# Optimization experiments

Measured on AMD Instinct MI355X. Metric: run time of the kernel, lower is better.

Reference implementation:

```python
import jax, jax.numpy as jnp
import numpy as np
from jax.scipy.special import logsumexp

EPS = 1e-12  # torch F.normalize eps
SINKHORN_ITERS = 3


def _l2norm(a, axis):
    n = jnp.sqrt(jnp.sum(a * a, axis=axis, keepdims=True))
    return a / jnp.maximum(n, EPS)


def _log_optimal_transport(scores, alpha, iters):
    # scores: [B, m, n]; alpha: scalar dust-bin param
    b, m, n = scores.shape
    bins = jnp.broadcast_to(alpha, (b, 1, n)).astype(scores.dtype)
    Z = jnp.concatenate([scores, bins], axis=1)  # [B, m+1, n]
    norm = -np.log(float(m + n))
    log_mu = jnp.asarray(
        np.concatenate([np.full(m, norm), [np.log(float(n - m)) + norm]]),
        scores.dtype,
    )  # [m+1]
    log_nu = jnp.full((n,), norm, scores.dtype)
    u = jnp.zeros((b, m + 1), scores.dtype)
    v = jnp.zeros((b, n), scores.dtype)
    for _ in range(iters):
        u = log_mu[None, :] - logsumexp(Z + v[:, None, :], axis=2)
        v = log_nu[None, :] - logsumexp(Z + u[:, :, None], axis=1)
    return Z + u[:, :, None] + v[:, None, :] - norm


def _forward(x, t, tw1, tb1, tw2, tb2, cw1, cb1, cw2, cb2, sw1, sb1, sw2, sb2, dust_bin):
    B, C = x.shape[0], x.shape[1]
    xf = x.reshape(B, C, -1)  # [B, C, N], 1x1 convs act per-location
    # cluster features f: [B, l, N]
    h = jax.nn.relu(jnp.einsum('oc,bcn->bon', cw1, xf) + cb1[None, :, None])
    f = jnp.einsum('oc,bcn->bon', cw2, h) + cb2[None, :, None]
    # global token: [B, g]
    tok = jax.nn.relu(t @ tw1.T + tb1) @ tw2.T + tb2
    # assignment scores p: [B, m, N]
    hs = jax.nn.relu(jnp.einsum('oc,bcn->bon', sw1, xf) + sb1[None, :, None])
    p = jnp.einsum('oc,bcn->bon', sw2, hs) + sb2[None, :, None]
    Z = _log_optimal_transport(p, dust_bin, SINKHORN_ITERS)
    P = jnp.exp(Z)[:, :-1, :]  # drop dust bin row -> [B, m, N]
    # VLAD-style aggregation: the repeat/multiply/sum is just a batched matmul
    agg = jnp.einsum('bln,bmn->blm', f, P)  # [B, l, m]
    agg = _l2norm(agg, axis=1).reshape(B, -1)  # intra-normalize over l, flatten l-major
    out = jnp.concatenate([_l2norm(tok, axis=-1), agg], axis=-1)
    return _l2norm(out, axis=-1)


def setup_inputs() -> dict:
    key = jax.random.key(0)
    ks = jax.random.split(key, 14)
    B, C, H, W = 64, 768, 32, 32
    L, M, G, HID = 128, 64, 256, 512

    def p(k, shape):
        return jax.random.normal(k, shape, jnp.float32) * 0.02

    return {
        'x': jax.random.normal(ks[0], (B, C, H, W), jnp.float32),
        't': jax.random.normal(ks[1], (B, C), jnp.float32),
        'tw1': p(ks[2], (HID, C)), 'tb1': jnp.zeros((HID,), jnp.float32),
        'tw2': p(ks[3], (G, HID)), 'tb2': jnp.zeros((G,), jnp.float32),
        'cw1': p(ks[4], (HID, C)), 'cb1': jnp.zeros((HID,), jnp.float32),
        'cw2': p(ks[5], (L, HID)), 'cb2': jnp.zeros((L,), jnp.float32),
        'sw1': p(ks[6], (HID, C)), 'sb1': jnp.zeros((HID,), jnp.float32),
        'sw2': p(ks[7], (M, HID)), 'sb2': jnp.zeros((M,), jnp.float32),
        'dust_bin': jnp.asarray(1.0, jnp.float32),
    }


def reference(x, t, tw1, tb1, tw2, tb2, cw1, cb1, cw2, cb2, sw1, sb1, sw2, sb2, dust_bin):
    return _forward(x, t, tw1, tb1, tw2, tb2, cw1, cb1, cw2, cb2, sw1, sb1, sw2, sb2, dust_bin)
```

## Files before the change

### kernel.cpp

```cpp
#include <hip/hip_runtime.h>
#include <math.h>


#define B_SZ   64
#define C_IN   768
#define N_LOC  1024
#define HID    512
#define L_DIM  128
#define M_DIM  64
#define G_DIM  256

typedef unsigned short u16;
typedef __bf16 bf16x8 __attribute__((ext_vector_type(8)));
typedef float f32x4 __attribute__((ext_vector_type(4)));

typedef const __attribute__((address_space(1))) void* gptr_t;
typedef __attribute__((address_space(3))) void* sptr_t;

__device__ __forceinline__ void load_lds16(const void* g, void* l) {
    __builtin_amdgcn_global_load_lds((gptr_t)g, (sptr_t)l, 16, 0, 0);
}

__device__ __forceinline__ u16 f2bf(float f) {
    unsigned u = __float_as_uint(f);
    u += 0x7fffu + ((u >> 16) & 1u);
    return (u16)(u >> 16);
}
__device__ __forceinline__ float bf2f(u16 h) {
    return __uint_as_float(((unsigned)h) << 16);
}

__device__ __forceinline__ float waveReduceSum(float v) {
#pragma unroll
    for (int off = 32; off > 0; off >>= 1) v += __shfl_xor(v, off, 64);
    return v;
}

__global__ __launch_bounds__(256) void prep_weights(
        const float* __restrict__ cw1, const float* __restrict__ sw1,
        const float* __restrict__ cw2, const float* __restrict__ sw2,
        u16* __restrict__ cw1p, u16* __restrict__ sw1p,
        u16* __restrict__ cw2p, u16* __restrict__ sw2p) {
    const int q = blockIdx.x * 256 + threadIdx.x;
    const float* src;
    u16* dst;
    if (q < 98304) {
        int path = q / 49152, r = q % 49152;
        int kt = r / 2048, kc = (r / 512) & 3, c = r & 511;
        src = (path ? sw1 : cw1) + (size_t)c * C_IN + kt * 32 + kc * 8;
        dst = (path ? sw1p : cw1p) + (size_t)r * 8;
    } else {
        int q2 = q - 98304;
        int path = (q2 >= 8192) ? 1 : 0;
        int r = q2 - (path ? 8192 : 0);
        int S2 = path ? M_DIM : L_DIM;
        int k2 = r / (4 * S2), kc = (r / S2) & 3, c = r % S2;
        src = (path ? sw2 : cw2) + (size_t)c * HID + k2 * 32 + kc * 8;
        dst = (path ? sw2p : cw2p) + (size_t)r * 8;
    }
    float4 v0 = *(const float4*)(src);
    float4 v1 = *(const float4*)(src + 4);
    *(ushort4*)(dst) = make_ushort4(f2bf(v0.x), f2bf(v0.y), f2bf(v0.z), f2bf(v0.w));
    *(ushort4*)(dst + 4) = make_ushort4(f2bf(v1.x), f2bf(v1.y), f2bf(v1.z), f2bf(v1.w));
}

__global__ __launch_bounds__(256) void transpose_x(const float* __restrict__ x,
                                                   u16* __restrict__ xP) {
    __shared__ float tile[64][65];
    const int n0 = blockIdx.x * 64;
    const int c0 = blockIdx.y * 64;
    const size_t b = blockIdx.z;
    const float* xb = x + b * (size_t)(C_IN * N_LOC);
    u16* xpb = xP + b * (size_t)(N_LOC * C_IN);
    const int tid = threadIdx.x;

    const int jn = (tid & 15) * 4;
    const int cr = tid >> 4;
#pragma unroll
    for (int r = 0; r < 4; ++r) {
        int c = cr + r * 16;
        float4 v = *(const float4*)(xb + (size_t)(c0 + c) * N_LOC + n0 + jn);
        tile[c][jn + 0] = v.x;
        tile[c][jn + 1] = v.y;
        tile[c][jn + 2] = v.z;
        tile[c][jn + 3] = v.w;
    }
    __syncthreads();

    const int n = tid & 63;
    const int ch0 = tid >> 6;
    const int nG = n0 + n;
#pragma unroll
    for (int r = 0; r < 2; ++r) {
        const int ch = ch0 + r * 4;
        const int cG = c0 + ch * 8;
        u16* dst = xpb + (size_t)(nG >> 7) * (128 * C_IN) + (cG >> 5) * 4096 +
                   ((cG & 31) >> 3) * 1024 + (nG & 127) * 8;
        ushort4 o0 = make_ushort4(f2bf(tile[ch * 8 + 0][n]), f2bf(tile[ch * 8 + 1][n]),
                                  f2bf(tile[ch * 8 + 2][n]), f2bf(tile[ch * 8 + 3][n]));
        ushort4 o1 = make_ushort4(f2bf(tile[ch * 8 + 4][n]), f2bf(tile[ch * 8 + 5][n]),
                                  f2bf(tile[ch * 8 + 6][n]), f2bf(tile[ch * 8 + 7][n]));
        *(ushort4*)(dst) = o0;
        *(ushort4*)(dst + 4) = o1;
    }
}

__global__ __launch_bounds__(512, 2) void fused12(
        const u16* __restrict__ xP,
        const u16* __restrict__ cw1p, const float* __restrict__ cb1,
        const u16* __restrict__ cw2p, const float* __restrict__ cb2,
        const u16* __restrict__ sw1p, const float* __restrict__ sb1,
        const u16* __restrict__ sw2p, const float* __restrict__ sb2,
        u16* __restrict__ fT, u16* __restrict__ pT) {
    __shared__ __align__(16) u16 LDSu[65536];
    const int tid = threadIdx.x;
    const int lane = tid & 63;
    const int wid = tid >> 6;
    const int wr = wid >> 2;
    const int wc = wid & 3;

    const int id = blockIdx.x + 8 * blockIdx.y + 16 * blockIdx.z;
    const int nid = (id & 7) * 128 + (id >> 3);
    const int bx = nid & 7;
    const int path = (nid >> 3) & 1;
    const int bz = nid >> 4;
    const int r0 = bx * 128;

    const u16* W1p = path ? sw1p : cw1p;
    const float* B1 = path ? sb1 : cb1;
    const u16* W2p = path ? sw2p : cw2p;
    const float* B2 = path ? sb2 : cb2;
    u16* O2 = path ? pT : fT;
    const int S2 = path ? M_DIM : L_DIM;

    const u16* Ap = xP + (size_t)bz * N_LOC * C_IN + (size_t)bx * (128 * C_IN);

    f32x4 acc1[4][8];
#pragma unroll
    for (int mi = 0; mi < 4; ++mi)
#pragma unroll
        for (int ni = 0; ni < 8; ++ni)
            acc1[mi][ni] = (f32x4){0.f, 0.f, 0.f, 0.f};

    const int nk = C_IN / 32;

#define STG_A(db_, kt_)                                                        \
    load_lds16(Ap + (size_t)(kt_) * 4096 + tid * 8, &LDSu[(db_) * 4096 + tid * 8])
#define STG_B(db_, kt_)                                                        \
    do {                                                                       \
        _Pragma("unroll")                                                      \
        for (int j_ = 0; j_ < 4; ++j_)                                         \
            load_lds16(W1p + (size_t)(kt_) * 16384 + (size_t)(j_ * 512 + tid) * 8, \
                       &LDSu[8192 + (db_) * 16384 + (j_ * 512 + tid) * 8]);    \
    } while (0)

#define AV_PTR(db_, mi_)                                                       \
    ((const bf16x8*)&LDSu[(db_) * 4096 + (lane >> 4) * 1024 +                  \
                          (64 * wr + 16 * (mi_) + (lane & 15)) * 8])
#define BW_PTR(db_, ni_)                                                       \
    ((const bf16x8*)&LDSu[8192 + (db_) * 16384 + (lane >> 4) * 4096 +          \
                          (128 * wc + 16 * (ni_) + (lane & 15)) * 8])

#define PHASE_MID()                                                            \
    __builtin_amdgcn_s_barrier();                                              \
    asm volatile("s_waitcnt lgkmcnt(0)" ::: "memory");                         \
    __builtin_amdgcn_sched_barrier(0);                                         \
    __builtin_amdgcn_s_setprio(1)

#define PHASE_END()                                                            \
    __builtin_amdgcn_s_setprio(0);                                             \
    __builtin_amdgcn_sched_barrier(0);                                         \
    __builtin_amdgcn_s_barrier()

    STG_A(0, 0);
    STG_B(0, 0);
    STG_A(1, 1);
    asm volatile("s_waitcnt vmcnt(1)" ::: "memory");
    __builtin_amdgcn_s_barrier();

    for (int t = 0; t < nk; ++t) {
        const int db = t & 1;
        bf16x8 av[4], bwl[4], bwh[4];

#pragma unroll
        for (int mi = 0; mi < 4; ++mi) av[mi] = *AV_PTR(db, mi);
#pragma unroll
        for (int ni = 0; ni < 4; ++ni) bwl[ni] = *BW_PTR(db, ni);
        if (t + 1 < nk) STG_B(db ^ 1, t + 1);
        PHASE_MID();
#pragma unroll
        for (int mi = 0; mi < 4; ++mi)
#pragma unroll
            for (int ni = 0; ni < 4; ++ni)
                acc1[mi][ni] = __builtin_amdgcn_mfma_f32_16x16x32_bf16(
                    av[mi], bwl[ni], acc1[mi][ni], 0, 0, 0);
        PHASE_END();

#pragma unroll
        for (int ni = 0; ni < 4; ++ni) bwh[ni] = *BW_PTR(db, 4 + ni);
        if (t + 2 < nk) STG_A(db, t + 2);
        PHASE_MID();
#pragma unroll
        for (int mi = 0; mi < 4; ++mi)
#pragma unroll
            for (int ni = 0; ni < 4; ++ni)
                acc1[mi][4 + ni] = __builtin_amdgcn_mfma_f32_16x16x32_bf16(
                    av[mi], bwh[ni], acc1[mi][4 + ni], 0, 0, 0);
        __builtin_amdgcn_s_setprio(0);
        __builtin_amdgcn_sched_barrier(0);
        if (t + 2 < nk)
            asm volatile("s_waitcnt vmcnt(1)" ::: "memory");
        else
            asm volatile("s_waitcnt vmcnt(0)" ::: "memory");
        __builtin_amdgcn_s_barrier();
    }
#undef STG_A
#undef STG_B
#undef AV_PTR
#undef BW_PTR
#undef PHASE_MID
#undef PHASE_END

    {
        float bv1[8];
#pragma unroll
        for (int ni = 0; ni < 8; ++ni)
            bv1[ni] = B1[128 * wc + 16 * ni + (lane & 15)];
#pragma unroll
        for (int mi = 0; mi < 4; ++mi)
#pragma unroll
            for (int ni = 0; ni < 8; ++ni)
#pragma unroll
                for (int rr = 0; rr < 4; ++rr) {
                    int n = 64 * wr + 16 * mi + (lane >> 4) * 4 + rr;
                    int c = 128 * wc + 16 * ni + (lane & 15);
                    float v = fmaxf(acc1[mi][ni][rr] + bv1[ni], 0.f);
                    LDSu[(c >> 3) * 1024 + n * 8 + (c & 7)] = f2bf(v);
                }
    }
    __syncthreads();

    f32x4 acc2[4][2];
#pragma unroll
    for (int mi = 0; mi < 4; ++mi) {
        acc2[mi][0] = (f32x4){0.f, 0.f, 0.f, 0.f};
        acc2[mi][1] = (f32x4){0.f, 0.f, 0.f, 0.f};
    }
    const int c2base = (S2 == L_DIM) ? 32 * wc : 16 * wc;
    const int cA = c2base + (lane & 15);
    const int cB = c2base + 16 + (lane & 15);
    const int fb0 = (lane >> 4) * S2 + cA;
    const int fb1 = (lane >> 4) * S2 + cB;

    bf16x8 w0n = *(const bf16x8*)(W2p + (size_t)fb0 * 8);
    bf16x8 w1n = {};
    if (S2 == L_DIM) w1n = *(const bf16x8*)(W2p + (size_t)fb1 * 8);

    for (int k2 = 0; k2 < 16; ++k2) {
        bf16x8 w0 = w0n, w1 = w1n;
        if (k2 < 15) {
            w0n = *(const bf16x8*)(W2p + ((size_t)(k2 + 1) * 4 * S2 + fb0) * 8);
            if (S2 == L_DIM)
                w1n = *(const bf16x8*)(W2p + ((size_t)(k2 + 1) * 4 * S2 + fb1) * 8);
        }
        bf16x8 a2[4];
#pragma unroll
        for (int mi = 0; mi < 4; ++mi)
            a2[mi] = *(const bf16x8*)&LDSu[(k2 * 4 + (lane >> 4)) * 1024 +
                                           (64 * wr + 16 * mi + (lane & 15)) * 8];
#pragma unroll
        for (int mi = 0; mi < 4; ++mi) {
            acc2[mi][0] = __builtin_amdgcn_mfma_f32_16x16x32_bf16(
                a2[mi], w0, acc2[mi][0], 0, 0, 0);
            if (S2 == L_DIM)
                acc2[mi][1] = __builtin_amdgcn_mfma_f32_16x16x32_bf16(
                    a2[mi], w1, acc2[mi][1], 0, 0, 0);
        }
    }

    const float b20 = B2[cA];
    const float b21 = (S2 == L_DIM) ? B2[cB] : 0.f;
    u16* Ob = O2 + (size_t)bz * N_LOC * S2;
#pragma unroll
    for (int mi = 0; mi < 4; ++mi)
#pragma unroll
        for (int rr = 0; rr < 4; ++rr) {
            int row = r0 + 64 * wr + 16 * mi + (lane >> 4) * 4 + rr;
            Ob[(size_t)row * S2 + cA] = f2bf(acc2[mi][0][rr] + b20);
            if (S2 == L_DIM)
                Ob[(size_t)row * S2 + cB] = f2bf(acc2[mi][1][rr] + b21);
        }
}

__global__ __launch_bounds__(256) void tok1_kernel(const float* __restrict__ t,
                                                   const float* __restrict__ tw1,
                                                   const float* __restrict__ tb1,
                                                   float* __restrict__ hidb) {
    __shared__ __align__(16) float tl[C_IN];
    const int b = blockIdx.y;
    const int j0 = blockIdx.x * 64;
    const int tid = threadIdx.x;
    const int lane = tid & 63;
    const int wave = tid >> 6;
    for (int i = tid; i < C_IN; i += 256) tl[i] = t[(size_t)b * C_IN + i];
    __syncthreads();
    for (int j = wave; j < 64; j += 4) {
        const int row = j0 + j;
        const float4* wr = (const float4*)(tw1 + (size_t)row * C_IN);
        const float4* tr = (const float4*)tl;
        float s = 0.f;
#pragma unroll
        for (int q = 0; q < 3; ++q) {
            float4 wv = wr[lane + 64 * q];
            float4 tv = tr[lane + 64 * q];
            s += wv.x * tv.x + wv.y * tv.y + wv.z * tv.z + wv.w * tv.w;
        }
        s = waveReduceSum(s);
        if (lane == 0) hidb[(size_t)b * HID + row] = fmaxf(s + tb1[row], 0.f);
    }
}

__global__ __launch_bounds__(256) void tok2_kernel(const float* __restrict__ hidb,
                                                   const float* __restrict__ tw2,
                                                   const float* __restrict__ tb2,
                                                   float* __restrict__ tok) {
    __shared__ __align__(16) float hl[HID];
    const int b = blockIdx.y;
    const int g0 = blockIdx.x * 64;
    const int tid = threadIdx.x;
    const int lane = tid & 63;
    const int wave = tid >> 6;
    for (int i = tid; i < HID; i += 256) hl[i] = hidb[(size_t)b * HID + i];
    __syncthreads();
    for (int j = wave; j < 64; j += 4) {
        const int row = g0 + j;
        const float4* wr = (const float4*)(tw2 + (size_t)row * HID);
        const float4* hr = (const float4*)hl;
        float s = 0.f;
#pragma unroll
        for (int q = 0; q < 2; ++q) {
            float4 wv = wr[lane + 64 * q];
            float4 hv = hr[lane + 64 * q];
            s += wv.x * hv.x + wv.y * hv.y + wv.z * hv.z + wv.w * hv.w;
        }
        s = waveReduceSum(s);
        if (lane == 0) tok[(size_t)b * G_DIM + row] = s + tb2[row];
    }
}

__global__ __launch_bounds__(1024) void sinkhorn_kernel(const u16* __restrict__ pT,
                                                        const float* __restrict__ dust,
                                                        float* __restrict__ PT) {
    __shared__ u16 sp[M_DIM][N_LOC];
    __shared__ float u[M_DIM + 1];
    __shared__ float v[N_LOC];
    const int b = blockIdx.x;
    const int t = threadIdx.x;
    const int lane = t & 63;
    const int wave = t >> 6;
    const float alpha = dust[0];
    const float norm = -__logf(1088.f);
    const float logmu_main = norm;
    const float logmu_last = __logf(960.f) + norm;
    const float lognu = norm;

    const uint4* prow = (const uint4*)(pT + ((size_t)b * N_LOC + t) * M_DIM);
#pragma unroll
    for (int q = 0; q < 8; ++q) {
        uint4 ch = prow[q];
        sp[q * 8 + 0][t] = (u16)(ch.x);
        sp[q * 8 + 1][t] = (u16)(ch.x >> 16);
        sp[q * 8 + 2][t] = (u16)(ch.y);
        sp[q * 8 + 3][t] = (u16)(ch.y >> 16);
        sp[q * 8 + 4][t] = (u16)(ch.z);
        sp[q * 8 + 5][t] = (u16)(ch.z >> 16);
        sp[q * 8 + 6][t] = (u16)(ch.w);
        sp[q * 8 + 7][t] = (u16)(ch.w >> 16);
    }
    v[t] = 0.f;
    if (t < M_DIM + 1) u[t] = 0.f;
    __syncthreads();

    for (int it = 0; it < 3; ++it) {
        for (int m = wave; m < M_DIM + 1; m += 16) {
            float s = 0.f;
            if (m < M_DIM) {
#pragma unroll
                for (int q = 0; q < 16; ++q) {
                    int c = lane + 64 * q;
                    s += __expf(bf2f(sp[m][c]) + v[c]);
                }
            } else {
#pragma unroll
                for (int q = 0; q < 16; ++q) {
                    int c = lane + 64 * q;
                    s += __expf(alpha + v[c]);
                }
            }
            s = waveReduceSum(s);
            if (lane == 0) u[m] = ((m < M_DIM) ? logmu_main : logmu_last) - __logf(s);
        }
        __syncthreads();
        float s = 0.f;
#pragma unroll 8
        for (int m = 0; m < M_DIM; ++m) s += __expf(bf2f(sp[m][t]) + u[m]);
        s += __expf(alpha + u[M_DIM]);
        v[t] = lognu - __logf(s);
        __syncthreads();
    }

    const float vt = v[t];
    float* Prow = PT + ((size_t)b * N_LOC + t) * M_DIM;
#pragma unroll
    for (int m4 = 0; m4 < M_DIM; m4 += 4) {
        float4 o;
        o.x = __expf(bf2f(sp[m4 + 0][t]) + u[m4 + 0] + vt - norm);
        o.y = __expf(bf2f(sp[m4 + 1][t]) + u[m4 + 1] + vt - norm);
        o.z = __expf(bf2f(sp[m4 + 2][t]) + u[m4 + 2] + vt - norm);
        o.w = __expf(bf2f(sp[m4 + 3][t]) + u[m4 + 3] + vt - norm);
        *(float4*)(Prow + m4) = o;
    }
}

__global__ __launch_bounds__(256) void agg_kernel(const u16* __restrict__ fT,
                                                  const float* __restrict__ PT,
                                                  float* __restrict__ agg) {
    __shared__ float Fs[64][36];
    __shared__ float Ps[64][68];
    const int b = blockIdx.y;
    const int l0 = blockIdx.x * 32;
    const int tid = threadIdx.x;
    const u16* fb = fT + (size_t)b * N_LOC * L_DIM;
    const float* Pb = PT + (size_t)b * N_LOC * M_DIM;

    const int sn = tid >> 2;
    const int flc = (tid & 3) * 8;
    const int pmc = (tid & 3) * 16;
    const int tl = (tid >> 4) * 2;
    const int tm = (tid & 15) * 4;

    float acc[2][4] = {};

    for (int n0 = 0; n0 < N_LOC; n0 += 64) {
        __syncthreads();
        {
            uint4 ld = *(const uint4*)(fb + (size_t)(n0 + sn) * L_DIM + l0 + flc);
            Fs[sn][flc + 0] = bf2f((u16)(ld.x));
            Fs[sn][flc + 1] = bf2f((u16)(ld.x >> 16));
            Fs[sn][flc + 2] = bf2f((u16)(ld.y));
            Fs[sn][flc + 3] = bf2f((u16)(ld.y >> 16));
            Fs[sn][flc + 4] = bf2f((u16)(ld.z));
            Fs[sn][flc + 5] = bf2f((u16)(ld.z >> 16));
            Fs[sn][flc + 6] = bf2f((u16)(ld.w));
            Fs[sn][flc + 7] = bf2f((u16)(ld.w >> 16));
        }
#pragma unroll
        for (int i = 0; i < 4; ++i) {
            float4 vv = *(const float4*)(Pb + (size_t)(n0 + sn) * M_DIM + pmc + 4 * i);
            *(float4*)&Ps[sn][pmc + 4 * i] = vv;
        }
        __syncthreads();
#pragma unroll 8
        for (int nn = 0; nn < 64; ++nn) {
            float a0 = Fs[nn][tl];
            float a1 = Fs[nn][tl + 1];
            float4 p4 = *(const float4*)&Ps[nn][tm];
            acc[0][0] = fmaf(a0, p4.x, acc[0][0]);
            acc[0][1] = fmaf(a0, p4.y, acc[0][1]);
            acc[0][2] = fmaf(a0, p4.z, acc[0][2]);
            acc[0][3] = fmaf(a0, p4.w, acc[0][3]);
            acc[1][0] = fmaf(a1, p4.x, acc[1][0]);
            acc[1][1] = fmaf(a1, p4.y, acc[1][1]);
            acc[1][2] = fmaf(a1, p4.z, acc[1][2]);
            acc[1][3] = fmaf(a1, p4.w, acc[1][3]);
        }
    }

#pragma unroll
    for (int i = 0; i < 2; ++i) {
        float* dst = agg + ((size_t)b * L_DIM + l0 + tl + i) * M_DIM + tm;
        *(float4*)dst = make_float4(acc[i][0], acc[i][1], acc[i][2], acc[i][3]);
    }
}

__global__ __launch_bounds__(256) void final_kernel(const float* __restrict__ agg,
                                                    const float* __restrict__ tok,
                                                    float* __restrict__ out) {
    __shared__ __align__(16) float ag[L_DIM * M_DIM];
    __shared__ float rm[M_DIM];
    __shared__ float red[4];
    __shared__ float tk[G_DIM];
    const int b = blockIdx.x;
    const int tid = threadIdx.x;
    const int lane = tid & 63;
    const int wave = tid >> 6;
    const float EPS = 1e-12f;

    const float4* ab = (const float4*)(agg + (size_t)b * L_DIM * M_DIM);
    for (int e4 = tid; e4 < L_DIM * M_DIM / 4; e4 += 256) ((float4*)ag)[e4] = ab[e4];
    tk[tid] = tok[(size_t)b * G_DIM + tid];
    __syncthreads();

    if (tid < M_DIM) {
        float ss = 0.f;
#pragma unroll 8
        for (int l = 0; l < L_DIM; ++l) {
            float x = ag[l * M_DIM + tid];
            ss = fmaf(x, x, ss);
        }
        rm[tid] = 1.f / fmaxf(sqrtf(ss), EPS);
    }
    const float tv = tk[tid];
    float ssl = tv * tv;
    ssl = waveReduceSum(ssl);
    if (lane == 0) red[wave] = ssl;
    __syncthreads();
    const float stok = red[0] + red[1] + red[2] + red[3];
    const float rt = 1.f / fmaxf(sqrtf(stok), EPS);
    const float tn = tv * rt;

    float gs = tn * tn;
    for (int e = tid; e < L_DIM * M_DIM; e += 256) {
        float x = ag[e] * rm[e & (M_DIM - 1)];
        gs = fmaf(x, x, gs);
    }
    __syncthreads();
    gs = waveReduceSum(gs);
    if (lane == 0) red[wave] = gs;
    __syncthreads();
    const float G = red[0] + red[1] + red[2] + red[3];
    const float rg = 1.f / fmaxf(sqrtf(G), EPS);

    float* ob = out + (size_t)b * (G_DIM + L_DIM * M_DIM);
    ob[tid] = tn * rg;
    for (int e = tid; e < L_DIM * M_DIM; e += 256)
        ob[G_DIM + e] = ag[e] * rm[e & (M_DIM - 1)] * rg;
}

extern "C" void kernel_launch(void* const* d_in, const int* in_sizes, int n_in,
                              void* d_out, int out_size, void* d_ws, size_t ws_size,
                              hipStream_t stream) {
    const float* x    = (const float*)d_in[0];
    const float* t    = (const float*)d_in[1];
    const float* tw1  = (const float*)d_in[2];
    const float* tb1  = (const float*)d_in[3];
    const float* tw2  = (const float*)d_in[4];
    const float* tb2  = (const float*)d_in[5];
    const float* cw1  = (const float*)d_in[6];
    const float* cb1  = (const float*)d_in[7];
    const float* cw2  = (const float*)d_in[8];
    const float* cb2  = (const float*)d_in[9];
    const float* sw1  = (const float*)d_in[10];
    const float* sb1  = (const float*)d_in[11];
    const float* sw2  = (const float*)d_in[12];
    const float* sb2  = (const float*)d_in[13];
    const float* dust = (const float*)d_in[14];
    float* out = (float*)d_out;

    char* ws = (char*)d_ws;
    u16* xP    = (u16*)(ws);
    u16* fT    = (u16*)(ws + 100663296ull);
    u16* pT    = (u16*)(ws + 117440512ull);
    u16* cw1p  = (u16*)(ws + 125829120ull);
    u16* sw1p  = (u16*)(ws + 126615552ull);
    u16* cw2p  = (u16*)(ws + 127401984ull);
    u16* sw2p  = (u16*)(ws + 127533056ull);
    float* hidb = (float*)(ws + 127598592ull);
    float* PT     = (float*)(ws);
    float* tokbuf = (float*)(ws + 20971520ull);
    float* aggbuf = (float*)(ws + 25165824ull);

    prep_weights<<<432, 256, 0, stream>>>(cw1, sw1, cw2, sw2,
                                          cw1p, sw1p, cw2p, sw2p);
    transpose_x<<<dim3(N_LOC / 64, C_IN / 64, B_SZ), 256, 0, stream>>>(x, xP);

    fused12<<<dim3(8, 2, B_SZ), 512, 0, stream>>>(
        xP, cw1p, cb1, cw2p, cb2, sw1p, sb1, sw2p, sb2, fT, pT);

    tok1_kernel<<<dim3(HID / 64, B_SZ), 256, 0, stream>>>(t, tw1, tb1, hidb);
    tok2_kernel<<<dim3(G_DIM / 64, B_SZ), 256, 0, stream>>>(hidb, tw2, tb2, tokbuf);

    sinkhorn_kernel<<<B_SZ, 1024, 0, stream>>>(pT, dust, PT);
    agg_kernel<<<dim3(L_DIM / 32, B_SZ), 256, 0, stream>>>(fT, PT, aggbuf);
    final_kernel<<<B_SZ, 256, 0, stream>>>(aggbuf, tokbuf, out);
}
```

Measured before the change: 286.0 us.

## Triple-buffer GEMM weights, run Sinkhorn in exp domain, fuse aggregation with final norm

Three changes. The fused GEMM's weight tile staging goes from double to triple buffering, so the B tile for step t+2 is prefetched and the vmcnt waits are adjusted to match. Sinkhorn is rewritten in the exponential domain: scores are exponentiated once and stored as bf16, and each iteration uses multiplies and divides instead of expf/logf per element. The aggregation kernel and the final normalization kernel are merged into one 512-thread block per batch, which removes the intermediate aggregation buffer and one launch but cuts the aggregation grid from 256 blocks to 64 and may underuse the GPU.

```diff
diff --git a/kernel.cpp b/kernel.cpp
--- a/kernel.cpp
+++ b/kernel.cpp
@@ -146,19 +146,19 @@
 
 #define STG_A(db_, kt_)                                                        \
     load_lds16(Ap + (size_t)(kt_) * 4096 + tid * 8, &LDSu[(db_) * 4096 + tid * 8])
-#define STG_B(db_, kt_)                                                        \
+#define STG_B(bb_, kt_)                                                        \
     do {                                                                       \
         _Pragma("unroll")                                                      \
         for (int j_ = 0; j_ < 4; ++j_)                                         \
             load_lds16(W1p + (size_t)(kt_) * 16384 + (size_t)(j_ * 512 + tid) * 8, \
-                       &LDSu[8192 + (db_) * 16384 + (j_ * 512 + tid) * 8]);    \
+                       &LDSu[8192 + (bb_) * 16384 + (j_ * 512 + tid) * 8]);    \
     } while (0)
 
 #define AV_PTR(db_, mi_)                                                       \
     ((const bf16x8*)&LDSu[(db_) * 4096 + (lane >> 4) * 1024 +                  \
                           (64 * wr + 16 * (mi_) + (lane & 15)) * 8])
-#define BW_PTR(db_, ni_)                                                       \
-    ((const bf16x8*)&LDSu[8192 + (db_) * 16384 + (lane >> 4) * 4096 +          \
+#define BW_PTR(bb_, ni_)                                                       \
+    ((const bf16x8*)&LDSu[8192 + (bb_) * 16384 + (lane >> 4) * 4096 +          \
                           (128 * wc + 16 * (ni_) + (lane & 15)) * 8])
 
 #define PHASE_MID()                                                            \
@@ -175,18 +175,21 @@
     STG_A(0, 0);
     STG_B(0, 0);
     STG_A(1, 1);
-    asm volatile("s_waitcnt vmcnt(1)" ::: "memory");
+    STG_B(1, 1);
+    asm volatile("s_waitcnt vmcnt(5)" ::: "memory");
     __builtin_amdgcn_s_barrier();
 
     for (int t = 0; t < nk; ++t) {
         const int db = t & 1;
+        const int bc = t % 3;
+        const int bs = (bc + 2 >= 3) ? bc - 1 : bc + 2;
         bf16x8 av[4], bwl[4], bwh[4];
 
 #pragma unroll
         for (int mi = 0; mi < 4; ++mi) av[mi] = *AV_PTR(db, mi);
 #pragma unroll
-        for (int ni = 0; ni < 4; ++ni) bwl[ni] = *BW_PTR(db, ni);
-        if (t + 1 < nk) STG_B(db ^ 1, t + 1);
+        for (int ni = 0; ni < 4; ++ni) bwl[ni] = *BW_PTR(bc, ni);
+        if (t + 2 < nk) STG_B(bs, t + 2);
         PHASE_MID();
 #pragma unroll
         for (int mi = 0; mi < 4; ++mi)
@@ -197,7 +200,7 @@
         PHASE_END();
 
 #pragma unroll
-        for (int ni = 0; ni < 4; ++ni) bwh[ni] = *BW_PTR(db, 4 + ni);
+        for (int ni = 0; ni < 4; ++ni) bwh[ni] = *BW_PTR(bc, 4 + ni);
         if (t + 2 < nk) STG_A(db, t + 2);
         PHASE_MID();
 #pragma unroll
@@ -209,7 +212,7 @@
         __builtin_amdgcn_s_setprio(0);
         __builtin_amdgcn_sched_barrier(0);
         if (t + 2 < nk)
-            asm volatile("s_waitcnt vmcnt(1)" ::: "memory");
+            asm volatile("s_waitcnt vmcnt(5)" ::: "memory");
         else
             asm volatile("s_waitcnt vmcnt(0)" ::: "memory");
         __builtin_amdgcn_s_barrier();
@@ -352,17 +355,17 @@
                                                         const float* __restrict__ dust,
                                                         float* __restrict__ PT) {
     __shared__ u16 sp[M_DIM][N_LOC];
-    __shared__ float u[M_DIM + 1];
-    __shared__ float v[N_LOC];
+    __shared__ float eu[M_DIM + 1];
+    __shared__ float ev[N_LOC];
     const int b = blockIdx.x;
     const int t = threadIdx.x;
     const int lane = t & 63;
     const int wave = t >> 6;
     const float alpha = dust[0];
-    const float norm = -__logf(1088.f);
-    const float logmu_main = norm;
-    const float logmu_last = __logf(960.f) + norm;
-    const float lognu = norm;
+    const float Ea = __expf(alpha);
+    const float mu = 1.f / 1088.f;
+    const float mu64 = 960.f / 1088.f;
+    const float nu = 1.f / 1088.f;
 
     const uint4* prow = (const uint4*)(pT + ((size_t)b * N_LOC + t) * M_DIM);
 #pragma unroll
@@ -377,8 +380,10 @@
         sp[q * 8 + 6][t] = (u16)(ch.w);
         sp[q * 8 + 7][t] = (u16)(ch.w >> 16);
     }
-    v[t] = 0.f;
-    if (t < M_DIM + 1) u[t] = 0.f;
+#pragma unroll
+    for (int m = 0; m < M_DIM; ++m)
+        sp[m][t] = f2bf(__expf(bf2f(sp[m][t])));
+    ev[t] = 1.f;
     __syncthreads();
 
     for (int it = 0; it < 3; ++it) {
@@ -388,117 +393,104 @@
 #pragma unroll
                 for (int q = 0; q < 16; ++q) {
                     int c = lane + 64 * q;
-                    s += __expf(bf2f(sp[m][c]) + v[c]);
+                    s += bf2f(sp[m][c]) * ev[c];
                 }
             } else {
 #pragma unroll
                 for (int q = 0; q < 16; ++q) {
                     int c = lane + 64 * q;
-                    s += __expf(alpha + v[c]);
+                    s += ev[c];
                 }
+                s *= Ea;
             }
             s = waveReduceSum(s);
-            if (lane == 0) u[m] = ((m < M_DIM) ? logmu_main : logmu_last) - __logf(s);
+            if (lane == 0) eu[m] = ((m < M_DIM) ? mu : mu64) / s;
         }
         __syncthreads();
-        float s = 0.f;
+        float s = Ea * eu[M_DIM];
 #pragma unroll 8
-        for (int m = 0; m < M_DIM; ++m) s += __expf(bf2f(sp[m][t]) + u[m]);
-        s += __expf(alpha + u[M_DIM]);
-        v[t] = lognu - __logf(s);
+        for (int m = 0; m < M_DIM; ++m) s += bf2f(sp[m][t]) * eu[m];
+        ev[t] = nu / s;
         __syncthreads();
     }
 
-    const float vt = v[t];
+    const float evt = ev[t] * 1088.f;
     float* Prow = PT + ((size_t)b * N_LOC + t) * M_DIM;
 #pragma unroll
     for (int m4 = 0; m4 < M_DIM; m4 += 4) {
         float4 o;
-        o.x = __expf(bf2f(sp[m4 + 0][t]) + u[m4 + 0] + vt - norm);
-        o.y = __expf(bf2f(sp[m4 + 1][t]) + u[m4 + 1] + vt - norm);
-        o.z = __expf(bf2f(sp[m4 + 2][t]) + u[m4 + 2] + vt - norm);
-        o.w = __expf(bf2f(sp[m4 + 3][t]) + u[m4 + 3] + vt - norm);
+        o.x = bf2f(sp[m4 + 0][t]) * eu[m4 + 0] * evt;
+        o.y = bf2f(sp[m4 + 1][t]) * eu[m4 + 1] * evt;
+        o.z = bf2f(sp[m4 + 2][t]) * eu[m4 + 2] * evt;
+        o.w = bf2f(sp[m4 + 3][t]) * eu[m4 + 3] * evt;
         *(float4*)(Prow + m4) = o;
     }
 }
 
-__global__ __launch_bounds__(256) void agg_kernel(const u16* __restrict__ fT,
-                                                  const float* __restrict__ PT,
-                                                  float* __restrict__ agg) {
-    __shared__ float Fs[64][36];
-    __shared__ float Ps[64][68];
-    const int b = blockIdx.y;
-    const int l0 = blockIdx.x * 32;
-    const int tid = threadIdx.x;
-    const u16* fb = fT + (size_t)b * N_LOC * L_DIM;
-    const float* Pb = PT + (size_t)b * N_LOC * M_DIM;
-
-    const int sn = tid >> 2;
-    const int flc = (tid & 3) * 8;
-    const int pmc = (tid & 3) * 16;
-    const int tl = (tid >> 4) * 2;
-    const int tm = (tid & 15) * 4;
-
-    float acc[2][4] = {};
-
-    for (int n0 = 0; n0 < N_LOC; n0 += 64) {
-        __syncthreads();
-        {
-            uint4 ld = *(const uint4*)(fb + (size_t)(n0 + sn) * L_DIM + l0 + flc);
-            Fs[sn][flc + 0] = bf2f((u16)(ld.x));
-            Fs[sn][flc + 1] = bf2f((u16)(ld.x >> 16));
-            Fs[sn][flc + 2] = bf2f((u16)(ld.y));
-            Fs[sn][flc + 3] = bf2f((u16)(ld.y >> 16));
-            Fs[sn][flc + 4] = bf2f((u16)(ld.z));
-            Fs[sn][flc + 5] = bf2f((u16)(ld.z >> 16));
-            Fs[sn][flc + 6] = bf2f((u16)(ld.w));
-            Fs[sn][flc + 7] = bf2f((u16)(ld.w >> 16));
-        }
-#pragma unroll
-        for (int i = 0; i < 4; ++i) {
-            float4 vv = *(const float4*)(Pb + (size_t)(n0 + sn) * M_DIM + pmc + 4 * i);
-            *(float4*)&Ps[sn][pmc + 4 * i] = vv;
-        }
-        __syncthreads();
-#pragma unroll 8
-        for (int nn = 0; nn < 64; ++nn) {
-            float a0 = Fs[nn][tl];
-            float a1 = Fs[nn][tl + 1];
-            float4 p4 = *(const float4*)&Ps[nn][tm];
-            acc[0][0] = fmaf(a0, p4.x, acc[0][0]);
-            acc[0][1] = fmaf(a0, p4.y, acc[0][1]);
-            acc[0][2] = fmaf(a0, p4.z, acc[0][2]);
-            acc[0][3] = fmaf(a0, p4.w, acc[0][3]);
-            acc[1][0] = fmaf(a1, p4.x, acc[1][0]);
-            acc[1][1] = fmaf(a1, p4.y, acc[1][1]);
-            acc[1][2] = fmaf(a1, p4.z, acc[1][2]);
-            acc[1][3] = fmaf(a1, p4.w, acc[1][3]);
-        }
-    }
-
-#pragma unroll
-    for (int i = 0; i < 2; ++i) {
-        float* dst = agg + ((size_t)b * L_DIM + l0 + tl + i) * M_DIM + tm;
-        *(float4*)dst = make_float4(acc[i][0], acc[i][1], acc[i][2], acc[i][3]);
-    }
-}
-
-__global__ __launch_bounds__(256) void final_kernel(const float* __restrict__ agg,
-                                                    const float* __restrict__ tok,
-                                                    float* __restrict__ out) {
+__global__ __launch_bounds__(512) void agg_final_kernel(const u16* __restrict__ fT,
+                                                        const float* __restrict__ PT,
+                                                        const float* __restrict__ tok,
+                                                        float* __restrict__ out) {
+    __shared__ __align__(16) float Fs[64][L_DIM];
+    __shared__ __align__(16) float Ps[64][M_DIM];
     __shared__ __align__(16) float ag[L_DIM * M_DIM];
     __shared__ float rm[M_DIM];
-    __shared__ float red[4];
+    __shared__ float red[8];
     __shared__ float tk[G_DIM];
     const int b = blockIdx.x;
     const int tid = threadIdx.x;
     const int lane = tid & 63;
     const int wave = tid >> 6;
     const float EPS = 1e-12f;
-
-    const float4* ab = (const float4*)(agg + (size_t)b * L_DIM * M_DIM);
-    for (int e4 = tid; e4 < L_DIM * M_DIM / 4; e4 += 256) ((float4*)ag)[e4] = ab[e4];
-    tk[tid] = tok[(size_t)b * G_DIM + tid];
+    const u16* fb = fT + (size_t)b * N_LOC * L_DIM;
+    const float* Pb = PT + (size_t)b * N_LOC * M_DIM;
+    const int m0 = (tid & 15) * 4;
+    const int l0 = (tid >> 4) * 4;
+
+    if (tid < G_DIM) tk[tid] = tok[(size_t)b * G_DIM + tid];
+
+    float acc[4][4] = {};
+    for (int n0 = 0; n0 < N_LOC; n0 += 64) {
+        __syncthreads();
+#pragma unroll
+        for (int pass = 0; pass < 2; ++pass) {
+            int idx = pass * 512 + tid;
+            int nn = idx >> 4, cc = (idx & 15) * 8;
+            const u16* src = fb + (size_t)(n0 + nn) * L_DIM + cc;
+            ushort4 h0 = *(const ushort4*)(src);
+            ushort4 h1 = *(const ushort4*)(src + 4);
+            Fs[nn][cc + 0] = bf2f(h0.x); Fs[nn][cc + 1] = bf2f(h0.y);
+            Fs[nn][cc + 2] = bf2f(h0.z); Fs[nn][cc + 3] = bf2f(h0.w);
+            Fs[nn][cc + 4] = bf2f(h1.x); Fs[nn][cc + 5] = bf2f(h1.y);
+            Fs[nn][cc + 6] = bf2f(h1.z); Fs[nn][cc + 7] = bf2f(h1.w);
+        }
+#pragma unroll
+        for (int pass = 0; pass < 2; ++pass) {
+            int idx = pass * 512 + tid;
+            int nn = idx >> 4, cc = (idx & 15) * 4;
+            float4 vv = *(const float4*)(Pb + (size_t)(n0 + nn) * M_DIM + cc);
+            *(float4*)&Ps[nn][cc] = vv;
+        }
+        __syncthreads();
+#pragma unroll 8
+        for (int nn = 0; nn < 64; ++nn) {
+            float4 a = *(const float4*)(&Fs[nn][l0]);
+            float4 bb = *(const float4*)(&Ps[nn][m0]);
+            float av[4] = {a.x, a.y, a.z, a.w};
+            float bv[4] = {bb.x, bb.y, bb.z, bb.w};
+#pragma unroll
+            for (int i = 0; i < 4; ++i)
+#pragma unroll
+                for (int j = 0; j < 4; ++j)
+                    acc[i][j] = fmaf(av[i], bv[j], acc[i][j]);
+        }
+    }
+
+#pragma unroll
+    for (int i = 0; i < 4; ++i)
+#pragma unroll
+        for (int j = 0; j < 4; ++j)
+            ag[(l0 + i) * M_DIM + m0 + j] = acc[i][j];
     __syncthreads();
 
     if (tid < M_DIM) {
@@ -510,17 +502,19 @@
         }
         rm[tid] = 1.f / fmaxf(sqrtf(ss), EPS);
     }
-    const float tv = tk[tid];
+    const float tv = (tid < G_DIM) ? tk[tid] : 0.f;
     float ssl = tv * tv;
     ssl = waveReduceSum(ssl);
     if (lane == 0) red[wave] = ssl;
     __syncthreads();
-    const float stok = red[0] + red[1] + red[2] + red[3];
+    float stok = 0.f;
+#pragma unroll
+    for (int w = 0; w < 8; ++w) stok += red[w];
     const float rt = 1.f / fmaxf(sqrtf(stok), EPS);
     const float tn = tv * rt;
 
-    float gs = tn * tn;
-    for (int e = tid; e < L_DIM * M_DIM; e += 256) {
+    float gs = (tid < G_DIM) ? tn * tn : 0.f;
+    for (int e = tid; e < L_DIM * M_DIM; e += 512) {
         float x = ag[e] * rm[e & (M_DIM - 1)];
         gs = fmaf(x, x, gs);
     }
@@ -528,12 +522,14 @@
     gs = waveReduceSum(gs);
     if (lane == 0) red[wave] = gs;
     __syncthreads();
-    const float G = red[0] + red[1] + red[2] + red[3];
+    float G = 0.f;
+#pragma unroll
+    for (int w = 0; w < 8; ++w) G += red[w];
     const float rg = 1.f / fmaxf(sqrtf(G), EPS);
 
     float* ob = out + (size_t)b * (G_DIM + L_DIM * M_DIM);
-    ob[tid] = tn * rg;
-    for (int e = tid; e < L_DIM * M_DIM; e += 256)
+    if (tid < G_DIM) ob[tid] = tn * rg;
+    for (int e = tid; e < L_DIM * M_DIM; e += 512)
         ob[G_DIM + e] = ag[e] * rm[e & (M_DIM - 1)] * rg;
 }
 
@@ -568,7 +564,6 @@
     float* hidb = (float*)(ws + 127598592ull);
     float* PT     = (float*)(ws);
     float* tokbuf = (float*)(ws + 20971520ull);
-    float* aggbuf = (float*)(ws + 25165824ull);
 
     prep_weights<<<432, 256, 0, stream>>>(cw1, sw1, cw2, sw2,
                                           cw1p, sw1p, cw2p, sw2p);
@@ -581,6 +576,5 @@
     tok2_kernel<<<dim3(G_DIM / 64, B_SZ), 256, 0, stream>>>(hidb, tw2, tb2, tokbuf);
 
     sinkhorn_kernel<<<B_SZ, 1024, 0, stream>>>(pT, dust, PT);
-    agg_kernel<<<dim3(L_DIM / 32, B_SZ), 256, 0, stream>>>(fT, PT, aggbuf);
-    final_kernel<<<B_SZ, 256, 0, stream>>>(aggbuf, tokbuf, out);
-}
+    agg_final_kernel<<<B_SZ, 512, 0, stream>>>(fT, PT, tokbuf, out);
+}
```

Result: slower. 307.4 us (+7.5%).

## Double GEMM K-tile to 64 and run Sinkhorn in exp domain

Applied to the files above, without the earlier changes.

The fused 1x1-conv GEMM now stages K-tiles of 64 instead of 32. The weight and activation repacking layouts change to match, and LDS grows to hold double-buffered A and B tiles. The pipeline is simplified to prefetch the full next tile while computing the current one. This cuts loop iterations and barriers per K, at the cost of more shared memory and a full vmcnt(0) wait each iteration. Separately, Sinkhorn is reformulated with multiplicative scalings (exp of scores precomputed once, stored as bf16). This removes the per-iteration exp and log calls but risks precision and overflow, since there is no log-domain stabilisation.

```diff
diff --git a/kernel.cpp b/kernel.cpp
--- a/kernel.cpp
+++ b/kernel.cpp
@@ -46,8 +46,8 @@
     u16* dst;
     if (q < 98304) {
         int path = q / 49152, r = q % 49152;
-        int kt = r / 2048, kc = (r / 512) & 3, c = r & 511;
-        src = (path ? sw1 : cw1) + (size_t)c * C_IN + kt * 32 + kc * 8;
+        int kch = r / 512, c = r & 511;
+        src = (path ? sw1 : cw1) + (size_t)c * C_IN + kch * 8;
         dst = (path ? sw1p : cw1p) + (size_t)r * 8;
     } else {
         int q2 = q - 98304;
@@ -94,8 +94,8 @@
     for (int r = 0; r < 2; ++r) {
         const int ch = ch0 + r * 4;
         const int cG = c0 + ch * 8;
-        u16* dst = xpb + (size_t)(nG >> 7) * (128 * C_IN) + (cG >> 5) * 4096 +
-                   ((cG & 31) >> 3) * 1024 + (nG & 127) * 8;
+        u16* dst = xpb + (size_t)(nG >> 7) * (128 * C_IN) + (cG >> 3) * 1024 +
+                   (nG & 127) * 8;
         ushort4 o0 = make_ushort4(f2bf(tile[ch * 8 + 0][n]), f2bf(tile[ch * 8 + 1][n]),
                                   f2bf(tile[ch * 8 + 2][n]), f2bf(tile[ch * 8 + 3][n]));
         ushort4 o1 = make_ushort4(f2bf(tile[ch * 8 + 4][n]), f2bf(tile[ch * 8 + 5][n]),
@@ -112,7 +112,7 @@
         const u16* __restrict__ sw1p, const float* __restrict__ sb1,
         const u16* __restrict__ sw2p, const float* __restrict__ sb2,
         u16* __restrict__ fT, u16* __restrict__ pT) {
-    __shared__ __align__(16) u16 LDSu[65536];
+    __shared__ __align__(16) u16 LDSu[81920];
     const int tid = threadIdx.x;
     const int lane = tid & 63;
     const int wid = tid >> 6;
@@ -142,23 +142,29 @@
         for (int ni = 0; ni < 8; ++ni)
             acc1[mi][ni] = (f32x4){0.f, 0.f, 0.f, 0.f};
 
-    const int nk = C_IN / 32;
+    const int nk = C_IN / 64;
 
 #define STG_A(db_, kt_)                                                        \
-    load_lds16(Ap + (size_t)(kt_) * 4096 + tid * 8, &LDSu[(db_) * 4096 + tid * 8])
+    do {                                                                       \
+        _Pragma("unroll")                                                      \
+        for (int j_ = 0; j_ < 2; ++j_)                                         \
+            load_lds16(Ap + (size_t)(kt_) * 8192 + (size_t)(j_ * 512 + tid) * 8, \
+                       &LDSu[(db_) * 8192 + (j_ * 512 + tid) * 8]);            \
+    } while (0)
 #define STG_B(db_, kt_)                                                        \
     do {                                                                       \
         _Pragma("unroll")                                                      \
-        for (int j_ = 0; j_ < 4; ++j_)                                         \
-            load_lds16(W1p + (size_t)(kt_) * 16384 + (size_t)(j_ * 512 + tid) * 8, \
-                       &LDSu[8192 + (db_) * 16384 + (j_ * 512 + tid) * 8]);    \
+        for (int j_ = 0; j_ < 8; ++j_)                                         \
+            load_lds16(W1p + (size_t)(kt_) * 32768 + (size_t)(j_ * 512 + tid) * 8, \
+                       &LDSu[16384 + (db_) * 32768 + (j_ * 512 + tid) * 8]);   \
     } while (0)
 
-#define AV_PTR(db_, mi_)                                                       \
-    ((const bf16x8*)&LDSu[(db_) * 4096 + (lane >> 4) * 1024 +                  \
+#define AV_PTR(db_, kk_, mi_)                                                  \
+    ((const bf16x8*)&LDSu[(db_) * 8192 + ((kk_) * 4 + (lane >> 4)) * 1024 +    \
                           (64 * wr + 16 * (mi_) + (lane & 15)) * 8])
-#define BW_PTR(db_, ni_)                                                       \
-    ((const bf16x8*)&LDSu[8192 + (db_) * 16384 + (lane >> 4) * 4096 +          \
+#define BW_PTR(db_, kk_, ni_)                                                  \
+    ((const bf16x8*)&LDSu[16384 + (db_) * 32768 +                              \
+                          ((kk_) * 4 + (lane >> 4)) * 4096 +                   \
                           (128 * wc + 16 * (ni_) + (lane & 15)) * 8])
 
 #define PHASE_MID()                                                            \
@@ -174,44 +180,44 @@
 
     STG_A(0, 0);
     STG_B(0, 0);
-    STG_A(1, 1);
-    asm volatile("s_waitcnt vmcnt(1)" ::: "memory");
+    asm volatile("s_waitcnt vmcnt(0)" ::: "memory");
     __builtin_amdgcn_s_barrier();
 
     for (int t = 0; t < nk; ++t) {
         const int db = t & 1;
-        bf16x8 av[4], bwl[4], bwh[4];
-
-#pragma unroll
-        for (int mi = 0; mi < 4; ++mi) av[mi] = *AV_PTR(db, mi);
-#pragma unroll
-        for (int ni = 0; ni < 4; ++ni) bwl[ni] = *BW_PTR(db, ni);
-        if (t + 1 < nk) STG_B(db ^ 1, t + 1);
+        bf16x8 av[4], bw[8];
+
+#pragma unroll
+        for (int mi = 0; mi < 4; ++mi) av[mi] = *AV_PTR(db, 0, mi);
+#pragma unroll
+        for (int ni = 0; ni < 8; ++ni) bw[ni] = *BW_PTR(db, 0, ni);
+        if (t + 1 < nk) {
+            STG_B(db ^ 1, t + 1);
+            STG_A(db ^ 1, t + 1);
+        }
         PHASE_MID();
 #pragma unroll
         for (int mi = 0; mi < 4; ++mi)
 #pragma unroll
-            for (int ni = 0; ni < 4; ++ni)
+            for (int ni = 0; ni < 8; ++ni)
                 acc1[mi][ni] = __builtin_amdgcn_mfma_f32_16x16x32_bf16(
-                    av[mi], bwl[ni], acc1[mi][ni], 0, 0, 0);
+                    av[mi], bw[ni], acc1[mi][ni], 0, 0, 0);
         PHASE_END();
 
 #pragma unroll
-        for (int ni = 0; ni < 4; ++ni) bwh[ni] = *BW_PTR(db, 4 + ni);
-        if (t + 2 < nk) STG_A(db, t + 2);
+        for (int mi = 0; mi < 4; ++mi) av[mi] = *AV_PTR(db, 1, mi);
+#pragma unroll
+        for (int ni = 0; ni < 8; ++ni) bw[ni] = *BW_PTR(db, 1, ni);
         PHASE_MID();
 #pragma unroll
         for (int mi = 0; mi < 4; ++mi)
 #pragma unroll
-            for (int ni = 0; ni < 4; ++ni)
-                acc1[mi][4 + ni] = __builtin_amdgcn_mfma_f32_16x16x32_bf16(
-                    av[mi], bwh[ni], acc1[mi][4 + ni], 0, 0, 0);
+            for (int ni = 0; ni < 8; ++ni)
+                acc1[mi][ni] = __builtin_amdgcn_mfma_f32_16x16x32_bf16(
+                    av[mi], bw[ni], acc1[mi][ni], 0, 0, 0);
         __builtin_amdgcn_s_setprio(0);
         __builtin_amdgcn_sched_barrier(0);
-        if (t + 2 < nk)
-            asm volatile("s_waitcnt vmcnt(1)" ::: "memory");
-        else
-            asm volatile("s_waitcnt vmcnt(0)" ::: "memory");
+        asm volatile("s_waitcnt vmcnt(0)" ::: "memory");
         __builtin_amdgcn_s_barrier();
     }
 #undef STG_A
@@ -352,17 +358,17 @@
                                                         const float* __restrict__ dust,
                                                         float* __restrict__ PT) {
     __shared__ u16 sp[M_DIM][N_LOC];
-    __shared__ float u[M_DIM + 1];
-    __shared__ float v[N_LOC];
+    __shared__ float eu[M_DIM + 1];
+    __shared__ float ev[N_LOC];
     const int b = blockIdx.x;
     const int t = threadIdx.x;
     const int lane = t & 63;
     const int wave = t >> 6;
     const float alpha = dust[0];
-    const float norm = -__logf(1088.f);
-    const float logmu_main = norm;
-    const float logmu_last = __logf(960.f) + norm;
-    const float lognu = norm;
+    const float Ea = __expf(alpha);
+    const float mu = 1.f / 1088.f;
+    const float mu64 = 960.f / 1088.f;
+    const float nu = 1.f / 1088.f;
 
     const uint4* prow = (const uint4*)(pT + ((size_t)b * N_LOC + t) * M_DIM);
 #pragma unroll
@@ -377,8 +383,10 @@
         sp[q * 8 + 6][t] = (u16)(ch.w);
         sp[q * 8 + 7][t] = (u16)(ch.w >> 16);
     }
-    v[t] = 0.f;
-    if (t < M_DIM + 1) u[t] = 0.f;
+#pragma unroll
+    for (int m = 0; m < M_DIM; ++m)
+        sp[m][t] = f2bf(__expf(bf2f(sp[m][t])));
+    ev[t] = 1.f;
     __syncthreads();
 
     for (int it = 0; it < 3; ++it) {
@@ -388,36 +396,36 @@
 #pragma unroll
                 for (int q = 0; q < 16; ++q) {
                     int c = lane + 64 * q;
-                    s += __expf(bf2f(sp[m][c]) + v[c]);
+                    s += bf2f(sp[m][c]) * ev[c];
                 }
             } else {
 #pragma unroll
                 for (int q = 0; q < 16; ++q) {
                     int c = lane + 64 * q;
-                    s += __expf(alpha + v[c]);
+                    s += ev[c];
                 }
+                s *= Ea;
             }
             s = waveReduceSum(s);
-            if (lane == 0) u[m] = ((m < M_DIM) ? logmu_main : logmu_last) - __logf(s);
+            if (lane == 0) eu[m] = ((m < M_DIM) ? mu : mu64) / s;
         }
         __syncthreads();
-        float s = 0.f;
+        float s = Ea * eu[M_DIM];
 #pragma unroll 8
-        for (int m = 0; m < M_DIM; ++m) s += __expf(bf2f(sp[m][t]) + u[m]);
-        s += __expf(alpha + u[M_DIM]);
-        v[t] = lognu - __logf(s);
+        for (int m = 0; m < M_DIM; ++m) s += bf2f(sp[m][t]) * eu[m];
+        ev[t] = nu / s;
         __syncthreads();
     }
 
-    const float vt = v[t];
+    const float evt = ev[t] * 1088.f;
     float* Prow = PT + ((size_t)b * N_LOC + t) * M_DIM;
 #pragma unroll
     for (int m4 = 0; m4 < M_DIM; m4 += 4) {
         float4 o;
-        o.x = __expf(bf2f(sp[m4 + 0][t]) + u[m4 + 0] + vt - norm);
-        o.y = __expf(bf2f(sp[m4 + 1][t]) + u[m4 + 1] + vt - norm);
-        o.z = __expf(bf2f(sp[m4 + 2][t]) + u[m4 + 2] + vt - norm);
-        o.w = __expf(bf2f(sp[m4 + 3][t]) + u[m4 + 3] + vt - norm);
+        o.x = bf2f(sp[m4 + 0][t]) * eu[m4 + 0] * evt;
+        o.y = bf2f(sp[m4 + 1][t]) * eu[m4 + 1] * evt;
+        o.z = bf2f(sp[m4 + 2][t]) * eu[m4 + 2] * evt;
+        o.w = bf2f(sp[m4 + 3][t]) * eu[m4 + 3] * evt;
         *(float4*)(Prow + m4) = o;
     }
 }
```

Result: no change. 291.5 us (+1.9%).
